# Optimization experiments

Hardware: AMD Instinct MI355X
Metric: run time of the kernel (lower is better)

## Reference

```python
import jax, jax.numpy as jnp
import numpy as np

HEADS = 8
EPS = 1e-12  # F.normalize default eps


def conv1x1(t, w):
    # t: (B, Cin, H, W); w: (Cout, Cin) -> (B, Cout, H, W)
    return jnp.einsum('bchw,oc->bohw', t, w)


def cosine_attn(q, k, v, scale):
    # q: (B,h,d,Nq); k,v: (B,h,d,Nk). Cosine attention: L2-normalize over feature dim d.
    q = q / jnp.maximum(jnp.linalg.norm(q, axis=2, keepdims=True), EPS)
    k = k / jnp.maximum(jnp.linalg.norm(k, axis=2, keepdims=True), EPS)
    attn = jnp.einsum('bhdq,bhdk->bhqk', q, k) * scale
    attn = jax.nn.softmax(attn, axis=-1)
    return jnp.einsum('bhqk,bhdk->bhdq', attn, v)  # (B,h,d,Nq)


def setup_inputs() -> dict:
    key = jax.random.key(0)
    ks = jax.random.split(key, 8)
    B, C, H, W, L = 8, 512, 64, 64, 16
    def w(k, o, i):
        return jax.random.normal(k, (o, i), dtype=jnp.float32) * (1.0 / np.sqrt(i))
    return {
        'x': jax.random.normal(ks[0], (B, C, H, W), dtype=jnp.float32),
        'latents': jax.random.normal(ks[1], (1, C, 1, L), dtype=jnp.float32) * 0.02,
        'w_q_lat': w(ks[2], C, C),
        'w_kv_x': w(ks[3], 2 * C, C),
        'w_q_x': w(ks[4], C, C),
        'w_kv_lat': w(ks[5], 2 * C, C),
        'w_proj': w(ks[6], C, C),
        'b_proj': jnp.zeros((C,), dtype=jnp.float32),
    }


def reference(x, latents, w_q_lat, w_kv_x, w_q_x, w_kv_lat, w_proj, b_proj):
    B, C, H, W = x.shape
    L = latents.shape[-1]
    h = HEADS
    d = C // h
    scale = d ** (-0.5)

    # latents read from spatial features (compression)
    lat = jnp.broadcast_to(latents, (B, C, 1, L))
    ql = conv1x1(lat, w_q_lat).reshape(B, h, d, L)
    kvx = conv1x1(x, w_kv_x)
    kx = kvx[:, :C].reshape(B, h, d, H * W)
    vx = kvx[:, C:].reshape(B, h, d, H * W)
    lat_read = cosine_attn(ql, kx, vx, scale).reshape(B, C, 1, L)

    # latents write back into features (expansion)
    qx = conv1x1(x, w_q_x).reshape(B, h, d, H * W)
    kvl = conv1x1(lat_read, w_kv_lat)
    kl = kvl[:, :C].reshape(B, h, d, L)
    vl = kvl[:, C:].reshape(B, h, d, L)
    x_write = cosine_attn(qx, kl, vl, scale).reshape(B, C, H, W)

    # output projection (dropout p=0 -> identity)
    return conv1x1(x_write, w_proj) + b_proj[None, :, None, None]
```

## Files before the change

kernel.cpp:

```cpp
#include <hip/hip_runtime.h>


typedef __bf16 bf16x8 __attribute__((ext_vector_type(8)));
typedef float floatx4 __attribute__((ext_vector_type(4)));
typedef short short8_t __attribute__((ext_vector_type(8)));
typedef short short4_t __attribute__((ext_vector_type(4)));

#define DEV __device__ __forceinline__

DEV float bf2f(unsigned short u){ union{unsigned int i; float f;} v; v.i = ((unsigned int)u)<<16; return v.f; }
DEV unsigned short f2bf(float f){
  __bf16 h = (__bf16)f;
  unsigned short u; __builtin_memcpy(&u, &h, 2); return u;
}

DEV void glds16(const void* g, void* l){
  __builtin_amdgcn_global_load_lds((const __attribute__((address_space(1))) void*)g,
                                   (__attribute__((address_space(3))) void*)l, 16, 0, 0);
}

#define OFF_XT     256ull
#define OFF_KVX    (OFF_XT + 33554432ull)
#define OFF_WKVX   (OFF_KVX + 67108864ull)
#define OFF_WQX    (OFF_WKVX + 1048576ull)
#define OFF_WKVL   (OFF_WQX + 524288ull)
#define OFF_WPROJ  (OFF_WKVL + 1048576ull)
#define OFF_WQLAT  (OFF_WPROJ + 524288ull)
#define OFF_LATF   (OFF_WQLAT + 524288ull)
#define OFF_BIAS   (OFF_LATF + 32768ull)
#define OFF_QLH    (OFF_BIAS + 4096ull)
#define OFF_GNUM   (OFF_QLH + 32768ull)
#define OFF_GDEN   (OFF_GNUM + 524288ull)
#define OFF_KVL    (OFF_GDEN + 4096ull)
#define OFF_KHAT   (OFF_KVL + 524288ull)
#define OFF_GVL    (OFF_KHAT + 524288ull)

__global__ void k_sniff(const unsigned short* __restrict__ x, int* flag){
  int t = threadIdx.x;
  int m = 0;
  for (int i = t; i < 4096; i += 256){ int e = (x[i]>>7)&0xFF; m = (e>m)?e:m; }
  __shared__ int red[256];
  red[t] = m; __syncthreads();
  for (int s = 128; s > 0; s >>= 1){ if (t < s) red[t] = (red[t+s]>red[t])?red[t+s]:red[t]; __syncthreads(); }
  if (t == 0) flag[0] = (red[0] > 150) ? 1 : 0;
}

__global__ __launch_bounds__(256) void k_prep(const void* s0, const void* s1, const void* s2,
                                              const void* s3, const void* s4,
                                              const void* slat, const void* sbias,
                                              unsigned short* __restrict__ wdst,
                                              float* __restrict__ latf, float* __restrict__ biasf,
                                              float* __restrict__ zro,
                                              const int* __restrict__ flag){
  int b = blockIdx.x, t = threadIdx.x;
  int isf = *flag;
  if (b < 896){
    int e = b*2048 + t*8;
    const void* src; int off;
    if (e < 524288)      { src = s0; off = e; }
    else if (e < 786432) { src = s1; off = e - 524288; }
    else if (e < 1310720){ src = s2; off = e - 786432; }
    else if (e < 1572864){ src = s3; off = e - 1310720; }
    else                 { src = s4; off = e - 1572864; }
    if (isf){
      const float* s = (const float*)src + off;
      float4 v0 = *(const float4*)(s);
      float4 v1 = *(const float4*)(s+4);
      unsigned short tmp[8] __attribute__((aligned(16)));
      tmp[0]=f2bf(v0.x); tmp[1]=f2bf(v0.y); tmp[2]=f2bf(v0.z); tmp[3]=f2bf(v0.w);
      tmp[4]=f2bf(v1.x); tmp[5]=f2bf(v1.y); tmp[6]=f2bf(v1.z); tmp[7]=f2bf(v1.w);
      *(short8_t*)&wdst[e] = *(short8_t*)tmp;
    } else {
      *(short8_t*)&wdst[e] = *(const short8_t*)((const unsigned short*)src + off);
    }
  } else if (b < 900){
    int i = (b-896)*2048 + t*8;
#pragma unroll
    for (int j = 0; j < 8; ++j)
      latf[i+j] = isf ? ((const float*)slat)[i+j] : bf2f(((const unsigned short*)slat)[i+j]);
  } else if (b == 900){
    if (t < 512) biasf[t] = isf ? ((const float*)sbias)[t] : bf2f(((const unsigned short*)sbias)[t]);
    if (t + 256 < 512) biasf[t+256] = isf ? ((const float*)sbias)[t+256] : bf2f(((const unsigned short*)sbias)[t+256]);
  } else {
    int i = (b-901)*256 + t;
    float4 z; z.x=0.f; z.y=0.f; z.z=0.f; z.w=0.f;
    ((float4*)zro)[i] = z;
  }
}

__global__ __launch_bounds__(256) void k_xt(const void* __restrict__ xraw, unsigned short* __restrict__ xT,
                                            const int* __restrict__ flag){
  int nb = blockIdx.x, cb = blockIdx.y, b = blockIdx.z;
  int n0 = nb*64, c0 = cb*64;
  __shared__ unsigned short tile[64][72];
  int t = threadIdx.x;
  if (*flag){
    const float* xp = (const float*)xraw;
#pragma unroll
    for (int i = 0; i < 4; ++i){
      int ch = i*256 + t; int c = ch>>4, n4 = (ch&15)*4;
      float4 v = *(const float4*)&xp[((size_t)(b*512 + c0 + c))*4096 + n0 + n4];
      int cc = n4 ^ (((c>>3)&7)<<3);
      tile[c][cc+0]=f2bf(v.x); tile[c][cc+1]=f2bf(v.y); tile[c][cc+2]=f2bf(v.z); tile[c][cc+3]=f2bf(v.w);
    }
  } else {
    const unsigned short* xp = (const unsigned short*)xraw;
#pragma unroll
    for (int i = 0; i < 2; ++i){
      int ch = i*256 + t; int c = ch>>3, n8 = (ch&7)*8;
      *(short8_t*)&tile[c][n8 ^ (((c>>3)&7)<<3)] =
        *(const short8_t*)&xp[((size_t)(b*512 + c0 + c))*4096 + n0 + n8];
    }
  }
  __syncthreads();
#pragma unroll
  for (int i = 0; i < 2; ++i){
    int ch = i*256 + t; int n = ch>>3, c8 = (ch&7)*8;
    unsigned short tmp[8] __attribute__((aligned(16)));
#pragma unroll
    for (int j = 0; j < 8; ++j){
      int c = c8 + j;
      tmp[j] = tile[c][n ^ (((c>>3)&7)<<3)];
    }
    *(short8_t*)&xT[((size_t)(b*4096 + n0 + n))*512 + c0 + c8] = *(short8_t*)tmp;
  }
}

__global__ __launch_bounds__(256) void k_ql(const unsigned short* __restrict__ wqlat,
                                            const float* __restrict__ latf, float* __restrict__ qlh){
  int h = blockIdx.x, o0 = h*64;
  extern __shared__ char smr[];
  float* latb = (float*)smr;
  unsigned short* wt = (unsigned short*)(smr + 8192);
  float* qbuf = (float*)(smr + 8192 + 17408);
  float* rinv = (float*)(smr + 8192 + 17408 + 4096);
  int t = threadIdx.x;
  int o = t>>2, l4 = (t&3)*4;
  float acc[4] = {0.f,0.f,0.f,0.f};
  for (int kk = 0; kk < 512; kk += 128){
    __syncthreads();
#pragma unroll
    for (int j = 0; j < 8; ++j){ int i = j*256 + t; latb[i] = latf[kk*16 + i]; }
#pragma unroll
    for (int j = 0; j < 4; ++j){ int ch = j*256 + t; int r = ch>>4, kc = (ch&15)*8;
      *(short8_t*)&wt[r*136 + kc] = *(const short8_t*)&wqlat[(size_t)(o0+r)*512 + kk + kc]; }
    __syncthreads();
    for (int k = 0; k < 128; ++k){
      float w = bf2f(wt[o*136 + k]);
      const float* lr = &latb[k*16 + l4];
#pragma unroll
      for (int j = 0; j < 4; ++j) acc[j] += w*lr[j];
    }
  }
#pragma unroll
  for (int j = 0; j < 4; ++j) qbuf[o*16 + l4 + j] = acc[j];
  __syncthreads();
  if (t < 16){
    float ss = 0.f;
    for (int oo = 0; oo < 64; ++oo){ float v = qbuf[oo*16 + t]; ss += v*v; }
    rinv[t] = 0.125f / fmaxf(sqrtf(ss), 1e-12f);
  }
  __syncthreads();
#pragma unroll
  for (int j = 0; j < 4; ++j) qlh[(h*16 + l4 + j)*64 + o] = acc[j]*rinv[l4 + j];
}

DEV void stage_ab8(const unsigned short* __restrict__ Ap0, const unsigned short* __restrict__ Ap1,
                   const unsigned short* __restrict__ Bp, int kk,
                   unsigned short* At, unsigned short* Bt, int wave, int rsub, int koff){
  if (wave < 4){
#pragma unroll
    for (int c2 = 0; c2 < 4; ++c2){
      int chunk = wave*4 + c2;
      int row = chunk*8 + rsub;
      const unsigned short* gp = (chunk < 8) ? (Ap0 + (size_t)row*512 + kk + koff)
                                             : (Ap1 + (size_t)(row-64)*512 + kk + koff);
      glds16(gp, At + chunk*512);
    }
  } else {
#pragma unroll
    for (int c2 = 0; c2 < 4; ++c2){
      int chunk = (wave-4)*4 + c2;
      int row = chunk*8 + rsub;
      glds16(Bp + (size_t)row*512 + kk + koff, Bt + chunk*512);
    }
  }
}

DEV void gemm128_db8(const unsigned short* __restrict__ Ap0, const unsigned short* __restrict__ Ap1,
                     const unsigned short* __restrict__ Bp,
                     char* smr, floatx4 (&acc)[4][2]){
  unsigned short* At0 = (unsigned short*)smr;
  unsigned short* Bt0 = (unsigned short*)(smr + 16384);
  unsigned short* At1 = (unsigned short*)(smr + 32768);
  unsigned short* Bt1 = (unsigned short*)(smr + 49152);
  int t = threadIdx.x, lane = t&63, wave = t>>6;
  int wm = wave&1, wn = wave>>1, lr = lane&15, lq = lane>>4;
  int rsub = lane>>3;
  int koff = ((lane&7) ^ rsub)*8;
  int sw = lr&7;
  stage_ab8(Ap0, Ap1, Bp, 0, At0, Bt0, wave, rsub, koff);
  __syncthreads();
  for (int kk = 0; kk < 512; kk += 64){
    int cur = (kk>>6)&1;
    unsigned short* Ac = cur ? At1 : At0;
    unsigned short* Bc = cur ? Bt1 : Bt0;
    if (kk < 448){
      stage_ab8(Ap0, Ap1, Bp, kk+64, cur ? At0 : At1, cur ? Bt0 : Bt1, wave, rsub, koff);
    }
    __builtin_amdgcn_s_setprio(1);
#pragma unroll
    for (int ks = 0; ks < 2; ++ks){
      int vo = ((ks*4 + lq) ^ sw)*8;
      bf16x8 a[4], b[2];
#pragma unroll
      for (int mt = 0; mt < 4; ++mt) a[mt] = *(const bf16x8*)&Ac[(wm*64 + mt*16 + lr)*64 + vo];
#pragma unroll
      for (int nt = 0; nt < 2; ++nt) b[nt] = *(const bf16x8*)&Bc[(wn*32 + nt*16 + lr)*64 + vo];
#pragma unroll
      for (int mt = 0; mt < 4; ++mt)
#pragma unroll
        for (int nt = 0; nt < 2; ++nt)
          acc[mt][nt] = __builtin_amdgcn_mfma_f32_16x16x32_bf16(a[mt], b[nt], acc[mt][nt], 0, 0, 0);
    }
    __builtin_amdgcn_s_setprio(0);
    __syncthreads();
  }
}

__global__ __launch_bounds__(512) void k_kvattn1(const unsigned short* __restrict__ wkvx,
                                                 const unsigned short* __restrict__ xT,
                                                 const float* __restrict__ qlh2,
                                                 float* __restrict__ gnum, float* __restrict__ gden){
  int nb = blockIdx.x, h = blockIdx.y, b = blockIdx.z;
  int n0 = nb*128;
  extern __shared__ char smr[];
  unsigned short* kt  = (unsigned short*)smr;
  unsigned short* vt  = (unsigned short*)(smr + 18432);
  unsigned short* pt  = (unsigned short*)(smr + 35840);
  unsigned short* qls = (unsigned short*)(smr + 65536);
  float* wred = (float*)(smr + 67840);
  int t = threadIdx.x, lane = t&63, wave = t>>6;
  int wm = wave&1, wn = wave>>1, lr = lane&15, lq = lane>>4;
  for (int i = t; i < 1024; i += 512) qls[(i>>6)*72 + (i&63)] = f2bf(qlh2[(size_t)h*1024 + i]);
  floatx4 acc[4][2];
  floatx4 zero = {0.f,0.f,0.f,0.f};
#pragma unroll
  for (int i = 0; i < 4; ++i) for (int j = 0; j < 2; ++j) acc[i][j] = zero;
  gemm128_db8(wkvx + (size_t)(h*64)*512, wkvx + (size_t)(512 + h*64)*512,
              xT + ((size_t)(b*4096 + n0))*512, smr, acc);
  if (wm == 0){
#pragma unroll
    for (int nt = 0; nt < 2; ++nt){
      float s = 0.f;
#pragma unroll
      for (int mt = 0; mt < 4; ++mt)
#pragma unroll
        for (int r = 0; r < 4; ++r) s += acc[mt][nt][r]*acc[mt][nt][r];
      s += __shfl_xor(s, 16); s += __shfl_xor(s, 32);
      float rinv = 1.f / fmaxf(sqrtf(s), 1e-12f);
      int col = wn*32 + nt*16 + lr;
#pragma unroll
      for (int mt = 0; mt < 4; ++mt){
        unsigned short tmp[4] __attribute__((aligned(8)));
#pragma unroll
        for (int r = 0; r < 4; ++r) tmp[r] = f2bf(acc[mt][nt][r]*rinv);
        *(short4_t*)&kt[col*72 + mt*16 + lq*4] = *(short4_t*)tmp;
      }
    }
  } else {
#pragma unroll
    for (int mt = 0; mt < 4; ++mt)
#pragma unroll
      for (int nt = 0; nt < 2; ++nt){
        int col = wn*32 + nt*16 + lr;
#pragma unroll
        for (int r = 0; r < 4; ++r) vt[(mt*16 + lq*4 + r)*136 + col] = f2bf(acc[mt][nt][r]);
      }
  }
  __syncthreads();
  floatx4 sl = zero;
#pragma unroll
  for (int ks = 0; ks < 2; ++ks){
    bf16x8 bb = *(const bf16x8*)&qls[lr*72 + ks*32 + lq*8];
    bf16x8 aa = *(const bf16x8*)&kt[(wave*16 + lr)*72 + ks*32 + lq*8];
    sl = __builtin_amdgcn_mfma_f32_16x16x32_bf16(aa, bb, sl, 0, 0, 0);
  }
  float dp = 0.f;
  float pv[4];
#pragma unroll
  for (int r = 0; r < 4; ++r){ float p = __expf(sl[r]); pv[r] = p; dp += p; }
  dp += __shfl_xor(dp, 16); dp += __shfl_xor(dp, 32);
  if (lq == 0) wred[wave*16 + lr] = dp;
  {
    unsigned short tmp[4] __attribute__((aligned(8)));
#pragma unroll
    for (int r = 0; r < 4; ++r) tmp[r] = f2bf(pv[r]);
    *(short4_t*)&pt[lr*136 + wave*16 + lq*4] = *(short4_t*)tmp;
  }
  __syncthreads();
  int bh = b*8 + h;
  if (t < 16){
    float s = 0.f;
#pragma unroll
    for (int w = 0; w < 8; ++w) s += wred[w*16 + t];
    atomicAdd(&gden[bh*16 + t], s);
  }
  if (wave < 4){
    floatx4 nacc = zero;
#pragma unroll
    for (int ks = 0; ks < 4; ++ks){
      bf16x8 aa = *(const bf16x8*)&vt[(wave*16 + lr)*136 + ks*32 + lq*8];
      bf16x8 bb = *(const bf16x8*)&pt[lr*136 + ks*32 + lq*8];
      nacc = __builtin_amdgcn_mfma_f32_16x16x32_bf16(aa, bb, nacc, 0, 0, 0);
    }
    float* gp = &gnum[((size_t)bh*16 + lr)*64 + wave*16 + lq*4];
#pragma unroll
    for (int r = 0; r < 4; ++r) atomicAdd(&gp[r], nacc[r]);
  }
}

__global__ __launch_bounds__(256) void k_kvl(const unsigned short* __restrict__ wkvl,
                                             const float* __restrict__ gnum, const float* __restrict__ gden,
                                             float* __restrict__ kvl){
  int ob = blockIdx.x, b = blockIdx.y;
  extern __shared__ char smr[];
  float* latb = (float*)smr;
  unsigned short* wt = (unsigned short*)(smr + 32768);
  int t = threadIdx.x;
  for (int i = t; i < 8192; i += 256){
    int c = i>>4, l = i&15;
    int h = c>>6, d = c&63;
    int bh = b*8 + h;
    latb[i] = gnum[((size_t)(bh*16 + l))*64 + d] / gden[bh*16 + l];
  }
  int o = t>>4, l = t&15;
  int o0 = ob*16;
  float acc = 0.f;
  for (int kk = 0; kk < 512; kk += 128){
    __syncthreads();
    { int r = t>>4, kc = (t&15)*8;
      *(short8_t*)&wt[r*136 + kc] = *(const short8_t*)&wkvl[(size_t)(o0+r)*512 + kk + kc]; }
    __syncthreads();
    for (int k = 0; k < 128; ++k) acc += bf2f(wt[o*136 + k]) * latb[(kk+k)*16 + l];
  }
  kvl[((size_t)(b*1024 + o0 + o))*16 + l] = acc;
}

__global__ void k_klnorm(const float* __restrict__ kvl, float* __restrict__ khat, float* __restrict__ gvl){
  int l = blockIdx.x, h = blockIdx.y, b = blockIdx.z, d = threadIdx.x;
  float kl = kvl[((size_t)(b*1024 + h*64 + d))*16 + l];
  float vl = kvl[((size_t)(b*1024 + 512 + h*64 + d))*16 + l];
  float ss = kl*kl;
  for (int off = 32; off; off >>= 1) ss += __shfl_xor(ss, off);
  float inv = 0.125f / fmaxf(sqrtf(ss), 1e-12f);
  size_t o = ((size_t)((b*8+h)*16 + l))*64 + d;
  khat[o] = kl*inv;
  gvl[o] = vl;
}

__global__ __launch_bounds__(256) void k_mmat(const unsigned short* __restrict__ wproj,
                                              const float* __restrict__ gvl,
                                              unsigned short* __restrict__ Mg){
  int cb = blockIdx.x, h = blockIdx.y, b = blockIdx.z;
  __shared__ unsigned short wt[128*68];
  int t = threadIdx.x;
#pragma unroll
  for (int i = 0; i < 4; ++i){ int ch = i*256 + t; int c = ch>>3, d8 = (ch&7)*8;
    *(short8_t*)&wt[c*68 + d8] = *(const short8_t*)&wproj[(size_t)(cb*128 + c)*512 + h*64 + d8]; }
  int l = t&15, cq = t>>4;
  float v[64];
  const float* vp = &gvl[((size_t)(b*8+h)*16 + l)*64];
#pragma unroll
  for (int j = 0; j < 16; ++j){ float4 f = *(const float4*)&vp[j*4];
    v[j*4+0]=f.x; v[j*4+1]=f.y; v[j*4+2]=f.z; v[j*4+3]=f.w; }
  __syncthreads();
#pragma unroll
  for (int c8 = 0; c8 < 8; ++c8){
    int c = cq*8 + c8;
    float dot = 0.f;
#pragma unroll
    for (int d = 0; d < 64; ++d) dot += bf2f(wt[c*68 + d]) * v[d];
    Mg[((size_t)(b*512) + cb*128 + c)*128 + h*16 + l] = f2bf(dot);
  }
}

__global__ __launch_bounds__(512) void k_attn2p2(const unsigned short* __restrict__ wqx,
                                                 const unsigned short* __restrict__ xT,
                                                 const float* __restrict__ khatg,
                                                 unsigned short* __restrict__ Pg){
  int nb = blockIdx.x, hp = blockIdx.y, b = blockIdx.z;
  int n0 = nb*128;
  extern __shared__ char smr[];
  unsigned short* qt0 = (unsigned short*)smr;
  unsigned short* qt1 = (unsigned short*)(smr + 18432);
  unsigned short* khs = (unsigned short*)(smr + 65536);
  int t = threadIdx.x, lane = t&63, wave = t>>6;
  int wm = wave&1, wn = wave>>1, lr = lane&15, lq = lane>>4;
  for (int i = t; i < 2048; i += 512){
    int hh = i>>10, rem = i&1023;
    khs[hh*1152 + (rem>>6)*72 + (rem&63)] = f2bf(khatg[((size_t)(b*8 + hp*2 + hh))*1024 + rem]);
  }
  floatx4 acc[4][2];
  floatx4 zero = {0.f,0.f,0.f,0.f};
#pragma unroll
  for (int i = 0; i < 4; ++i) for (int j = 0; j < 2; ++j) acc[i][j] = zero;
  gemm128_db8(wqx + (size_t)(hp*128)*512, wqx + (size_t)(hp*128 + 64)*512,
              xT + ((size_t)(b*4096 + n0))*512, smr, acc);
  unsigned short* qtr = wm ? qt1 : qt0;
#pragma unroll
  for (int nt = 0; nt < 2; ++nt){
    float s = 0.f;
#pragma unroll
    for (int mt = 0; mt < 4; ++mt)
#pragma unroll
      for (int r = 0; r < 4; ++r) s += acc[mt][nt][r]*acc[mt][nt][r];
    s += __shfl_xor(s, 16); s += __shfl_xor(s, 32);
    float rinv = 1.f / fmaxf(sqrtf(s), 1e-12f);
    int col = wn*32 + nt*16 + lr;
#pragma unroll
    for (int mt = 0; mt < 4; ++mt){
      unsigned short tmp[4] __attribute__((aligned(8)));
#pragma unroll
      for (int r = 0; r < 4; ++r) tmp[r] = f2bf(acc[mt][nt][r]*rinv);
      *(short4_t*)&qtr[col*72 + mt*16 + lq*4] = *(short4_t*)tmp;
    }
  }
  __syncthreads();
  floatx4 sl[2];
  sl[0] = zero; sl[1] = zero;
  unsigned short* qsrc = wm ? qt1 : qt0;
#pragma unroll
  for (int ks = 0; ks < 2; ++ks){
    bf16x8 bb = *(const bf16x8*)&khs[wm*1152 + lr*72 + ks*32 + lq*8];
#pragma unroll
    for (int i = 0; i < 2; ++i){
      bf16x8 aa = *(const bf16x8*)&qsrc[((wn*2 + i)*16 + lr)*72 + ks*32 + lq*8];
      sl[i] = __builtin_amdgcn_mfma_f32_16x16x32_bf16(aa, bb, sl[i], 0, 0, 0);
    }
  }
  int h = hp*2 + wm;
#pragma unroll
  for (int i = 0; i < 2; ++i){
    float p[4], s[4];
#pragma unroll
    for (int r = 0; r < 4; ++r){ p[r] = __expf(sl[i][r]); s[r] = p[r]; }
#pragma unroll
    for (int r = 0; r < 4; ++r){
      s[r] += __shfl_xor(s[r], 1);
      s[r] += __shfl_xor(s[r], 2);
      s[r] += __shfl_xor(s[r], 4);
      s[r] += __shfl_xor(s[r], 8);
    }
    int nbase = wn*32 + i*16 + lq*4;
#pragma unroll
    for (int r = 0; r < 4; ++r)
      Pg[((size_t)(b*4096 + n0 + nbase + r))*128 + h*16 + lr] = f2bf(p[r]/s[r]);
  }
}

__global__ __launch_bounds__(256) void k_out(const unsigned short* __restrict__ Mg,
                                             const unsigned short* __restrict__ Pg,
                                             const float* __restrict__ biasf,
                                             void* __restrict__ outv, const int* __restrict__ flag){
  int nb = blockIdx.x, cb = blockIdx.y, b = blockIdx.z;
  int n0 = nb*128, c0 = cb*64;
  extern __shared__ char smr[];
  unsigned short* At = (unsigned short*)smr;
  unsigned short* Bt = At + 64*136;
  int t = threadIdx.x, lane = t&63, wave = t>>6;
  int wm = wave>>1, wn = wave&1, lr = lane&15, lq = lane>>4;
#pragma unroll
  for (int i = 0; i < 4; ++i){ int ch = i*256 + t; int r = ch>>4, p8 = (ch&15)*8;
    *(short8_t*)&At[r*136 + p8] = *(const short8_t*)&Mg[((size_t)(b*512 + c0 + r))*128 + p8]; }
#pragma unroll
  for (int i = 0; i < 8; ++i){ int ch = i*256 + t; int r = ch>>4, p8 = (ch&15)*8;
    *(short8_t*)&Bt[r*136 + p8] = *(const short8_t*)&Pg[((size_t)(b*4096 + n0 + r))*128 + p8]; }
  __syncthreads();
  floatx4 acc[2][4];
  floatx4 zero = {0.f,0.f,0.f,0.f};
#pragma unroll
  for (int i = 0; i < 2; ++i) for (int j = 0; j < 4; ++j) acc[i][j] = zero;
#pragma unroll
  for (int ks = 0; ks < 4; ++ks){
    bf16x8 a0 = *(const bf16x8*)&At[(wm*32 + lr)*136 + ks*32 + lq*8];
    bf16x8 a1 = *(const bf16x8*)&At[(wm*32 + 16 + lr)*136 + ks*32 + lq*8];
#pragma unroll
    for (int nt = 0; nt < 4; ++nt){
      bf16x8 bb = *(const bf16x8*)&Bt[(wn*64 + nt*16 + lr)*136 + ks*32 + lq*8];
      acc[0][nt] = __builtin_amdgcn_mfma_f32_16x16x32_bf16(a0, bb, acc[0][nt], 0, 0, 0);
      acc[1][nt] = __builtin_amdgcn_mfma_f32_16x16x32_bf16(a1, bb, acc[1][nt], 0, 0, 0);
    }
  }
  __syncthreads();
  float* ct = (float*)smr;
#pragma unroll
  for (int mt = 0; mt < 2; ++mt)
#pragma unroll
    for (int nt = 0; nt < 4; ++nt)
#pragma unroll
      for (int r = 0; r < 4; ++r){
        int row = wm*32 + mt*16 + lq*4 + r;
        ct[row*132 + wn*64 + nt*16 + lr] = acc[mt][nt][r] + biasf[c0 + row];
      }
  __syncthreads();
  if (*flag){
    float* of = (float*)outv;
#pragma unroll
    for (int i = 0; i < 8; ++i){ int ch = i*256 + t; int r = ch>>5, c4 = (ch&31)*4;
      *(float4*)&of[((size_t)(b*512 + c0 + r))*4096 + n0 + c4] = *(float4*)&ct[r*132 + c4]; }
  } else {
    unsigned short* ob = (unsigned short*)outv;
#pragma unroll
    for (int i = 0; i < 4; ++i){ int ch = i*256 + t; int r = ch>>4, c8 = (ch&15)*8;
      unsigned short tmp[8] __attribute__((aligned(16)));
#pragma unroll
      for (int j = 0; j < 8; ++j) tmp[j] = f2bf(ct[r*132 + c8 + j]);
      *(short8_t*)&ob[((size_t)(b*512 + c0 + r))*4096 + n0 + c8] = *(short8_t*)tmp; }
  }
}

extern "C" void kernel_launch(void* const* d_in, const int* in_sizes, int n_in,
                              void* d_out, int out_size, void* d_ws, size_t ws_size,
                              hipStream_t stream){
  (void)in_sizes; (void)n_in; (void)out_size; (void)ws_size;
  char* ws = (char*)d_ws;
  int* flag              = (int*)ws;
  unsigned short* xT     = (unsigned short*)(ws + OFF_XT);
  unsigned short* Pg     = (unsigned short*)(ws + OFF_KVX);
  unsigned short* Mg     = (unsigned short*)(ws + OFF_KVX + 8388608ull);
  unsigned short* wkvx   = (unsigned short*)(ws + OFF_WKVX);
  unsigned short* wqx    = (unsigned short*)(ws + OFF_WQX);
  unsigned short* wkvl   = (unsigned short*)(ws + OFF_WKVL);
  unsigned short* wproj  = (unsigned short*)(ws + OFF_WPROJ);
  float* latf  = (float*)(ws + OFF_LATF);
  float* biasf = (float*)(ws + OFF_BIAS);
  float* qlh   = (float*)(ws + OFF_QLH);
  float* gnum  = (float*)(ws + OFF_GNUM);
  float* gden  = (float*)(ws + OFF_GDEN);
  float* kvl   = (float*)(ws + OFF_KVL);
  float* khat  = (float*)(ws + OFF_KHAT);
  float* gvl   = (float*)(ws + OFF_GVL);

  k_sniff<<<1, 256, 0, stream>>>((const unsigned short*)d_in[0], flag);

  k_prep<<<1030, 256, 0, stream>>>(d_in[3], d_in[4], d_in[5], d_in[6], d_in[2],
                                   d_in[1], d_in[7], wkvx, latf, biasf, gnum, flag);

  k_xt<<<dim3(64, 8, 8), 256, 0, stream>>>(d_in[0], xT, flag);

  k_ql<<<8, 256, 8192 + 17408 + 4096 + 64, stream>>>((unsigned short*)(ws + OFF_WQLAT), latf, qlh);

  k_kvattn1<<<dim3(32, 8, 8), 512, 68352, stream>>>(wkvx, xT, qlh, gnum, gden);
  k_kvl<<<dim3(64, 8), 256, 32768 + 16*136*2, stream>>>(wkvl, gnum, gden, kvl);
  k_klnorm<<<dim3(16, 8, 8), 64, 0, stream>>>(kvl, khat, gvl);
  k_mmat<<<dim3(4, 8, 8), 256, 0, stream>>>(wproj, gvl, Mg);
  k_attn2p2<<<dim3(32, 4, 8), 512, 70144, stream>>>(wqx, xT, khat, Pg);
  k_out<<<dim3(32, 8, 8), 256, 52224, stream>>>(Mg, Pg, biasf, d_out, flag);
}
```

Measured before the change: 276.8 us.

## Replace double-buffered K=64 GEMM with triple-buffered K=32 pipeline in kvattn1

Replaces the kvattn1 GEMM mainloop with a three-stage ring of 32-wide K slices loaded through direct global-to-LDS copies, using explicit vmcnt waits and a single barrier per step. Shared memory for the kernel drops from about 68KB to about 52KB, which may allow more resident blocks per CU and hides load latency with two stages in flight. In exchange there are more loop iterations and barriers, fewer MFMAs per barrier, and a new swizzle that must avoid LDS bank conflicts.

```diff
diff --git a/kernel.cpp b/kernel.cpp
--- a/kernel.cpp
+++ b/kernel.cpp
@@ -228,6 +228,67 @@
   }
 }
 
+DEV void stage32(const unsigned short* __restrict__ Ap0, const unsigned short* __restrict__ Ap1,
+                 const unsigned short* __restrict__ Bp, int kk,
+                 char* buf, int wave, int rsub, int koff){
+  if (wave < 4){
+#pragma unroll
+    for (int j = 0; j < 2; ++j){
+      int c = wave*2 + j;
+      int row = c*16 + rsub;
+      const unsigned short* gp = (c < 4) ? (Ap0 + (size_t)row*512 + kk + koff)
+                                         : (Ap1 + (size_t)(row-64)*512 + kk + koff);
+      glds16(gp, buf + c*1024);
+    }
+  } else {
+#pragma unroll
+    for (int j = 0; j < 2; ++j){
+      int c = (wave-4)*2 + j;
+      int row = c*16 + rsub;
+      glds16(Bp + (size_t)row*512 + kk + koff, buf + 8192 + c*1024);
+    }
+  }
+}
+
+DEV void gemm32_tri(const unsigned short* __restrict__ Ap0, const unsigned short* __restrict__ Ap1,
+                    const unsigned short* __restrict__ Bp,
+                    char* smr, floatx4 (&acc)[4][2]){
+  int t = threadIdx.x, lane = t&63, wave = t>>6;
+  int wm = wave&1, wn = wave>>1, lr = lane&15, lq = lane>>4;
+  int rsub = lane>>2;
+  int koff = ((lane&3) ^ ((lane>>3)&3))*8;
+  int sw2 = (lr>>1)&3;
+  char* p0 = smr;
+  char* p1 = smr + 16384;
+  char* p2 = smr + 32768;
+  stage32(Ap0, Ap1, Bp, 0,  p0, wave, rsub, koff);
+  stage32(Ap0, Ap1, Bp, 32, p1, wave, rsub, koff);
+  for (int k = 0; k < 16; ++k){
+    if (k == 15) asm volatile("s_waitcnt vmcnt(0)" ::: "memory");
+    else         asm volatile("s_waitcnt vmcnt(2)" ::: "memory");
+    __builtin_amdgcn_sched_barrier(0);
+    __builtin_amdgcn_s_barrier();
+    if (k < 14) stage32(Ap0, Ap1, Bp, (k+2)*32, p2, wave, rsub, koff);
+    __builtin_amdgcn_s_setprio(1);
+    int vo = (lq ^ sw2)*8;
+    const unsigned short* A = (const unsigned short*)p0;
+    const unsigned short* B = (const unsigned short*)(p0 + 8192);
+    bf16x8 a[4], b[2];
+#pragma unroll
+    for (int mt = 0; mt < 4; ++mt) a[mt] = *(const bf16x8*)&A[(wm*64 + mt*16 + lr)*32 + vo];
+#pragma unroll
+    for (int nt = 0; nt < 2; ++nt) b[nt] = *(const bf16x8*)&B[(wn*32 + nt*16 + lr)*32 + vo];
+#pragma unroll
+    for (int mt = 0; mt < 4; ++mt)
+#pragma unroll
+      for (int nt = 0; nt < 2; ++nt)
+        acc[mt][nt] = __builtin_amdgcn_mfma_f32_16x16x32_bf16(a[mt], b[nt], acc[mt][nt], 0, 0, 0);
+    __builtin_amdgcn_s_setprio(0);
+    char* tmp = p0; p0 = p1; p1 = p2; p2 = tmp;
+  }
+  __syncthreads();
+}
+
 __global__ __launch_bounds__(512) void k_kvattn1(const unsigned short* __restrict__ wkvx,
                                                  const unsigned short* __restrict__ xT,
                                                  const float* __restrict__ qlh2,
@@ -238,8 +299,8 @@
   unsigned short* kt  = (unsigned short*)smr;
   unsigned short* vt  = (unsigned short*)(smr + 18432);
   unsigned short* pt  = (unsigned short*)(smr + 35840);
-  unsigned short* qls = (unsigned short*)(smr + 65536);
-  float* wred = (float*)(smr + 67840);
+  unsigned short* qls = (unsigned short*)(smr + 49152);
+  float* wred = (float*)(smr + 51456);
   int t = threadIdx.x, lane = t&63, wave = t>>6;
   int wm = wave&1, wn = wave>>1, lr = lane&15, lq = lane>>4;
   for (int i = t; i < 1024; i += 512) qls[(i>>6)*72 + (i&63)] = f2bf(qlh2[(size_t)h*1024 + i]);
@@ -247,8 +308,8 @@
   floatx4 zero = {0.f,0.f,0.f,0.f};
 #pragma unroll
   for (int i = 0; i < 4; ++i) for (int j = 0; j < 2; ++j) acc[i][j] = zero;
-  gemm128_db8(wkvx + (size_t)(h*64)*512, wkvx + (size_t)(512 + h*64)*512,
-              xT + ((size_t)(b*4096 + n0))*512, smr, acc);
+  gemm32_tri(wkvx + (size_t)(h*64)*512, wkvx + (size_t)(512 + h*64)*512,
+             xT + ((size_t)(b*4096 + n0))*512, smr, acc);
   if (wm == 0){
 #pragma unroll
     for (int nt = 0; nt < 2; ++nt){
@@ -551,7 +612,7 @@
 
   k_ql<<<8, 256, 8192 + 17408 + 4096 + 64, stream>>>((unsigned short*)(ws + OFF_WQLAT), latf, qlh);
 
-  k_kvattn1<<<dim3(32, 8, 8), 512, 68352, stream>>>(wkvx, xT, qlh, gnum, gden);
+  k_kvattn1<<<dim3(32, 8, 8), 512, 51968, stream>>>(wkvx, xT, qlh, gnum, gden);
   k_kvl<<<dim3(64, 8), 256, 32768 + 16*136*2, stream>>>(wkvl, gnum, gden, kvl);
   k_klnorm<<<dim3(16, 8, 8), 64, 0, stream>>>(kvl, khat, gvl);
   k_mmat<<<dim3(4, 8, 8), 256, 0, stream>>>(wproj, gvl, Mg);
```

Result: no change. 278.4 us (+0.6%).
